# Performance work log

Hardware: AMD Instinct MI355X
Metric: run time of the kernel (lower is better)

The kernel has to match this reference:

```python
import jax, jax.numpy as jnp
import numpy as np

B, S, H = 8, 2048, 1024
NH, HD, NS, K = 16, 64, 64, 4  # num_heads, head_dim, state_size, conv kernel


def setup_inputs() -> dict:
    key = jax.random.key(0)
    ks = jax.random.split(key, 16)
    sc = 0.02
    return {
        "x": jax.random.normal(ks[0], (B, S, H), dtype=jnp.float32),
        # weights stored (in, out) so y = x @ W + b
        "in_proj_w": jax.random.normal(ks[1], (H, 2 * H), dtype=jnp.float32) * sc,
        "conv_w": jax.random.normal(ks[2], (H, 1, K), dtype=jnp.float32) * sc,
        "conv_b": jnp.zeros((H,), dtype=jnp.float32),
        "bb_w": jax.random.normal(ks[3], (HD, HD), dtype=jnp.float32) * sc,
        "bb_b": jnp.zeros((HD,), dtype=jnp.float32),
        "f1_w": jax.random.normal(ks[4], (HD, NS), dtype=jnp.float32) * sc,
        "f1_b": jnp.zeros((NS,), dtype=jnp.float32),
        "f2_w": jax.random.normal(ks[5], (HD, NS), dtype=jnp.float32) * sc,
        "f2_b": jnp.zeros((NS,), dtype=jnp.float32),
        "tau_a_w": jax.random.normal(ks[6], (HD, NS), dtype=jnp.float32) * sc,
        "tau_a_b": jnp.zeros((NS,), dtype=jnp.float32),
        "tau_b": jnp.zeros((NS,), dtype=jnp.float32),
        "decay_w": jax.random.normal(ks[7], (HD, NS), dtype=jnp.float32) * sc,
        "decay_b": jnp.zeros((NS,), dtype=jnp.float32),
        "state_out_w": jax.random.normal(ks[8], (NS, HD), dtype=jnp.float32) * sc,
        "state_out_b": jnp.zeros((HD,), dtype=jnp.float32),
        "out_proj_w": jax.random.normal(ks[9], (H, H), dtype=jnp.float32) * sc,
    }


def _short_conv(x, w, b):
    # x: (B,S,D) depthwise causal conv, kernel K, left-pad K-1
    xc = jnp.transpose(x, (0, 2, 1))  # (B,D,S)
    y = jax.lax.conv_general_dilated(
        xc, w, window_strides=(1,), padding=[(K - 1, 0)],
        feature_group_count=H, dimension_numbers=("NCH", "OIH", "NCH"))
    y = y + b[None, :, None]
    return jnp.transpose(y, (0, 2, 1))  # (B,S,D)


def _scan(decay, candidate):
    # decay, candidate: (B,S,NH,NS); h_t = d_t*h_{t-1} + (1-d_t)*c_t
    d = jnp.transpose(decay, (1, 0, 2, 3))      # (S,B,NH,NS)
    c = jnp.transpose(candidate, (1, 0, 2, 3))

    def step(h, dc):
        dt, ct = dc
        h = dt * h + (1.0 - dt) * ct
        return h, h

    h0 = jnp.zeros(d.shape[1:], dtype=decay.dtype)
    _, hs = jax.lax.scan(step, h0, (d, c))
    return jnp.transpose(hs, (1, 0, 2, 3))      # (B,S,NH,NS)


def reference(x, in_proj_w, conv_w, conv_b, bb_w, bb_b, f1_w, f1_b,
              f2_w, f2_b, tau_a_w, tau_a_b, tau_b, decay_w, decay_b,
              state_out_w, state_out_b, out_proj_w):
    xz = x @ in_proj_w                       # (B,S,2H)
    x_path, z_gate = jnp.split(xz, 2, axis=-1)
    x_path = jax.nn.silu(_short_conv(x_path, conv_w, conv_b))
    x_heads = x_path.reshape(B, S, NH, HD)
    bb = jax.nn.silu(x_heads @ bb_w + bb_b)  # backbone (1 layer)
    f1 = jnp.tanh(bb @ f1_w + f1_b)
    f2 = jnp.tanh(bb @ f2_w + f2_b)
    tau = jax.nn.sigmoid(bb @ tau_a_w + tau_a_b + tau_b)
    candidate = f1 * (1.0 - tau) + f2 * tau
    decay = jax.nn.sigmoid(bb @ decay_w + decay_b)
    h_seq = _scan(decay, candidate)          # (B,S,NH,NS)
    out = h_seq @ state_out_w + state_out_b  # (B,S,NH,HD)
    out = out.reshape(B, S, H)
    out = out * jax.nn.silu(z_gate)
    return out @ out_proj_w
```

## Files before the change

### kernel.cpp

```cpp
#include <hip/hip_runtime.h>
#include <hip/hip_bf16.h>
#include <math.h>

#define BN   8
#define SN   2048
#define HN   1024
#define NTOK 16384
#define NHD  16
#define HDD  64
#define NSD  64

typedef __attribute__((ext_vector_type(8))) short short8;
typedef __attribute__((ext_vector_type(4))) float f32x4;

__device__ __forceinline__ float fsig(float x)  { return 1.f / (1.f + __expf(-x)); }
__device__ __forceinline__ float fsilu(float x) { return x / (1.f + __expf(-x)); }
__device__ __forceinline__ float ftanh(float x) {
    const float t = __expf(-2.f * fabsf(x));
    const float r = (1.f - t) / (1.f + t);
    return x >= 0.f ? r : -r;
}
__device__ __forceinline__ void hilo(float v, __hip_bfloat16& h, __hip_bfloat16& l) {
    h = __float2bfloat16(v);
    l = __float2bfloat16(v - __bfloat162float(h));
}
__device__ __forceinline__ unsigned pack_cd(float cand, float dec) {
    __hip_bfloat16 cb_ = __float2bfloat16(cand);
    __hip_bfloat16 db_ = __float2bfloat16(dec);
    return (unsigned)*(unsigned short*)&cb_ | ((unsigned)*(unsigned short*)&db_ << 16);
}
__device__ __forceinline__ void gload_lds16(const void* g, void* l) {
    __builtin_amdgcn_global_load_lds(
        (const __attribute__((address_space(1))) unsigned int*)g,
        (__attribute__((address_space(3))) unsigned int*)l, 16, 0, 0);
}

__global__ __launch_bounds__(256)
void x_to_a_bf(const float* __restrict__ X, __hip_bfloat16* __restrict__ A)
{
    const int idx = blockIdx.x * 256 + threadIdx.x;
    const int r = idx >> 7;
    const int c = idx & 127;
    const float* src = &X[(size_t)r * 1024 + c * 8];
    alignas(16) __hip_bfloat16 b[8];
#pragma unroll
    for (int j = 0; j < 8; ++j) b[j] = __float2bfloat16(src[j]);
    const int cs = (c & 120) | ((c & 7) ^ (r & 7));
    *(short8*)&A[(size_t)r * 1024 + cs * 8] = *(const short8*)b;
}

__global__ __launch_bounds__(256)
void w_to_bt_bf(const float* __restrict__ W, __hip_bfloat16* __restrict__ BT, int N)
{
    __shared__ float t[64][65];
    const int k0 = blockIdx.x * 64;
    const int n0 = blockIdx.y * 64;
    const int c  = threadIdx.x & 63, r4 = threadIdx.x >> 6;
#pragma unroll
    for (int rr = 0; rr < 64; rr += 4)
        t[rr + r4][c] = W[(size_t)(k0 + rr + r4) * N + n0 + c];
    __syncthreads();
#pragma unroll
    for (int oo = 0; oo < 2; ++oo) {
        const int o = r4 * 2 + oo;
        alignas(16) __hip_bfloat16 b[8];
#pragma unroll
        for (int j = 0; j < 8; ++j)
            b[j] = __float2bfloat16(t[o * 8 + j][c]);
        const int n = n0 + c;
        const int cglob = (k0 >> 3) + o;
        const int cs = (cglob & 120) | ((cglob & 7) ^ (n & 7));
        *(short8*)&BT[(size_t)n * 1024 + cs * 8] = *(const short8*)b;
    }
}

__global__ __launch_bounds__(256)
void w5_to_wt(const float* __restrict__ w0, const float* __restrict__ w1,
              const float* __restrict__ w2, const float* __restrict__ w3,
              const float* __restrict__ w4, __hip_bfloat16* __restrict__ WT5)
{
    const int idx = blockIdx.x * 256 + threadIdx.x;
    if (idx >= 2560) return;
    const int o = idx & 7, n = (idx >> 3) & 63, mat = idx >> 9;
    const float* W = mat == 0 ? w0 : mat == 1 ? w1 : mat == 2 ? w2 : mat == 3 ? w3 : w4;
    alignas(16) __hip_bfloat16 hb[8], lb[8];
#pragma unroll
    for (int j = 0; j < 8; ++j) {
        const float v = W[(o * 8 + j) * 64 + n];
        hilo(v, hb[j], lb[j]);
    }
    __hip_bfloat16* row = WT5 + (size_t)(mat * 64 + n) * 128;
    *(short8*)&row[((o     ) ^ (n & 15)) * 8] = *(const short8*)hb;
    *(short8*)&row[((o | 8) ^ (n & 15)) * 8] = *(const short8*)lb;
}

template<int NCT, int MODE>
__global__ __launch_bounds__(512, 2)
void mfma_gemm256(const __hip_bfloat16* __restrict__ A,
                  const __hip_bfloat16* __restrict__ BT,
                  float* __restrict__ out0, float* __restrict__ out1)
{
    __shared__ __hip_bfloat16 lds[2][2][16384];
    const int tid  = threadIdx.x;
    const int lane = tid & 63, wave = tid >> 6;
    const int wr   = wave >> 2, wc = wave & 3;
    const int l15  = lane & 15, l4 = lane >> 4;

    const int nwg = gridDim.x;
    const int cpx = nwg >> 3;
    const int swz = (blockIdx.x & 7) * cpx + (blockIdx.x >> 3);
    const int mt = swz / NCT, nt = swz % NCT;
    const int row0 = mt * 256, col0 = nt * 256;

    const int s_c = tid & 7;
    const int s_r = (tid >> 3) & 63;

    f32x4 acc[8][4];
#pragma unroll
    for (int m = 0; m < 8; ++m)
#pragma unroll
        for (int n = 0; n < 4; ++n) acc[m][n] = (f32x4)0.f;

#define STAGE_I(I, TT, BUF)                                                    \
    {                                                                          \
        const int mat_ = (I) >> 2;                                             \
        const int row_ = ((I) & 3) * 64 + s_r;                                 \
        const __hip_bfloat16* src_ = (mat_ == 0)                               \
            ? &A [(size_t)(row0 + row_) * 1024 + ((TT) << 6) + s_c * 8]        \
            : &BT[(size_t)(col0 + row_) * 1024 + ((TT) << 6) + s_c * 8];       \
        gload_lds16(src_, &lds[BUF][mat_][row_ * 64 + s_c * 8]);               \
    }

#pragma unroll
    for (int i = 0; i < 8; ++i) STAGE_I(i, 0, 0)
    __syncthreads();

    for (int t = 0; t < 16; ++t) {
        const int cur = t & 1, nxt = cur ^ 1;
        const bool pf = (t < 15);

#pragma unroll
        for (int ks = 0; ks < 2; ++ks) {
            if (pf) {
#pragma unroll
                for (int i = ks * 4; i < ks * 4 + 4; ++i) STAGE_I(i, t + 1, nxt)
            }

            short8 af[8], bf[4];
#pragma unroll
            for (int m = 0; m < 8; ++m) {
                const int row = wr * 128 + m * 16 + l15;
                const int ch = (ks * 4 + l4) ^ (l15 & 7);
                af[m] = *(const short8*)&lds[cur][0][row * 64 + ch * 8];
            }
#pragma unroll
            for (int n = 0; n < 4; ++n) {
                const int row = wc * 64 + n * 16 + l15;
                const int ch = (ks * 4 + l4) ^ (l15 & 7);
                bf[n] = *(const short8*)&lds[cur][1][row * 64 + ch * 8];
            }

            __builtin_amdgcn_s_setprio(1);
#pragma unroll
            for (int m = 0; m < 8; ++m)
#pragma unroll
                for (int n = 0; n < 4; ++n)
                    acc[m][n] = __builtin_amdgcn_mfma_f32_16x16x32_bf16(af[m], bf[n], acc[m][n], 0, 0, 0);
            __builtin_amdgcn_s_setprio(0);
        }
        __syncthreads();
    }
#undef STAGE_I

    const int orow = l4 * 4, ocol = l15;
#pragma unroll
    for (int M = 0; M < 8; ++M)
#pragma unroll
        for (int N = 0; N < 4; ++N) {
            const int c = col0 + wc * 64 + N * 16 + ocol;
#pragma unroll
            for (int q = 0; q < 4; ++q) {
                const int r = row0 + wr * 128 + M * 16 + orow + q;
                const float v = acc[M][N][q];
                if (MODE == 0) {
                    out0[(size_t)r * (NCT * 256) + c] = v;
                } else {
                    if (c < 1024) out0[(size_t)r * 1024 + c] = v;
                    else          out1[(size_t)r * 1024 + (c - 1024)] = fsilu(v);
                }
            }
        }
}

__global__ __launch_bounds__(512, 1)
void backbone_mfma(const float* __restrict__ xpath,
                   const float* __restrict__ cw, const float* __restrict__ cb,
                   const __hip_bfloat16* __restrict__ WT5,
                   const float* __restrict__ bbb,
                   const float* __restrict__ f1b, const float* __restrict__ f2b,
                   const float* __restrict__ taub, const float* __restrict__ taub2,
                   const float* __restrict__ decb,
                   unsigned* __restrict__ cd)
{
    __shared__ __hip_bfloat16 Wl[5 * 64 * 128];
    __shared__ __hip_bfloat16 Xl[128 * 128];
    __shared__ __hip_bfloat16 Bb[128 * 128];
    const int tid  = threadIdx.x;
    const int lane = tid & 63, wave = tid >> 6;
    const int l15  = lane & 15, l4 = lane >> 4;

#pragma unroll
    for (int r = 0; r < 10; ++r) {
        const int blk = r * 8 + wave;
        gload_lds16(WT5 + blk * 512 + lane * 8, Wl + blk * 512);
    }

    {
        const int bt = blockIdx.x * 8 + wave;
        const int t  = bt & (SN - 1);
#pragma unroll
        for (int gg = 0; gg < 2; ++gg) {
            const int g  = lane + gg * 64;
            const int c0 = g * 8;
            float acc[8];
#pragma unroll
            for (int j = 0; j < 8; ++j) acc[j] = cb[c0 + j];
            float4 cwv[8];
#pragma unroll
            for (int j = 0; j < 8; ++j) cwv[j] = *(const float4*)&cw[(c0 + j) * 4];
            const float* cwf = (const float*)cwv;
#pragma unroll
            for (int k = 0; k < 4; ++k) {
                if (t - 3 + k >= 0) {
                    const float* xr = xpath + (((size_t)(bt - 3 + k)) << 10) + c0;
                    const float4 u0 = *(const float4*)&xr[0];
                    const float4 u1 = *(const float4*)&xr[4];
                    const float u[8] = {u0.x, u0.y, u0.z, u0.w, u1.x, u1.y, u1.z, u1.w};
#pragma unroll
                    for (int j = 0; j < 8; ++j) acc[j] += cwf[j * 4 + k] * u[j];
                }
            }
            alignas(16) __hip_bfloat16 hb[8], lb[8];
#pragma unroll
            for (int j = 0; j < 8; ++j) hilo(fsilu(acc[j]), hb[j], lb[j]);
            const int head = c0 >> 6;
            const int o    = (c0 >> 3) & 7;
            __hip_bfloat16* row = Xl + (wave * 16 + head) * 128;
            *(short8*)&row[((o     ) ^ head) * 8] = *(const short8*)hb;
            *(short8*)&row[((o | 8) ^ head) * 8] = *(const short8*)lb;
        }
    }
    __syncthreads();

    short8 xa[2][2];
#pragma unroll
    for (int s = 0; s < 2; ++s)
#pragma unroll
        for (int p = 0; p < 2; ++p) {
            const int ch = ((s * 4 + l4) | (p << 3)) ^ l15;
            xa[s][p] = *(const short8*)&Xl[(wave * 16 + l15) * 128 + ch * 8];
        }

#pragma unroll
    for (int nt = 0; nt < 4; ++nt) {
        short8 wb[2][2];
#pragma unroll
        for (int s = 0; s < 2; ++s)
#pragma unroll
            for (int p = 0; p < 2; ++p) {
                const int ch = ((s * 4 + l4) | (p << 3)) ^ l15;
                wb[s][p] = *(const short8*)&Wl[(nt * 16 + l15) * 128 + ch * 8];
            }
        f32x4 ac = (f32x4)0.f;
        __builtin_amdgcn_s_setprio(1);
#pragma unroll
        for (int s = 0; s < 2; ++s) {
            ac = __builtin_amdgcn_mfma_f32_16x16x32_bf16(xa[s][0], wb[s][0], ac, 0, 0, 0);
            ac = __builtin_amdgcn_mfma_f32_16x16x32_bf16(xa[s][0], wb[s][1], ac, 0, 0, 0);
            ac = __builtin_amdgcn_mfma_f32_16x16x32_bf16(xa[s][1], wb[s][0], ac, 0, 0, 0);
        }
        __builtin_amdgcn_s_setprio(0);
        const int col = nt * 16 + l15;
        const float bc = bbb[col];
#pragma unroll
        for (int q = 0; q < 4; ++q) {
            const int r15 = l4 * 4 + q;
            const float v = fsilu(ac[q] + bc);
            __hip_bfloat16 h, l;
            hilo(v, h, l);
            Bb[(wave * 16 + r15) * 128 + (((col >> 3)     ) ^ r15) * 8 + (col & 7)] = h;
            Bb[(wave * 16 + r15) * 128 + (((col >> 3) | 8) ^ r15) * 8 + (col & 7)] = l;
        }
    }

    short8 ba[2][2];
#pragma unroll
    for (int s = 0; s < 2; ++s)
#pragma unroll
        for (int p = 0; p < 2; ++p) {
            const int ch = ((s * 4 + l4) | (p << 3)) ^ l15;
            ba[s][p] = *(const short8*)&Bb[(wave * 16 + l15) * 128 + ch * 8];
        }

#pragma unroll
    for (int nt = 0; nt < 4; ++nt) {
        f32x4 a2[4];
#pragma unroll
        for (int m = 0; m < 4; ++m) a2[m] = (f32x4)0.f;

#pragma unroll
        for (int mat = 0; mat < 4; ++mat) {
            short8 w2[2][2];
#pragma unroll
            for (int s = 0; s < 2; ++s)
#pragma unroll
                for (int p = 0; p < 2; ++p) {
                    const int ch = ((s * 4 + l4) | (p << 3)) ^ l15;
                    w2[s][p] = *(const short8*)&Wl[((mat + 1) * 64 + nt * 16 + l15) * 128 + ch * 8];
                }
            __builtin_amdgcn_s_setprio(1);
#pragma unroll
            for (int s = 0; s < 2; ++s) {
                a2[mat] = __builtin_amdgcn_mfma_f32_16x16x32_bf16(ba[s][0], w2[s][0], a2[mat], 0, 0, 0);
                a2[mat] = __builtin_amdgcn_mfma_f32_16x16x32_bf16(ba[s][0], w2[s][1], a2[mat], 0, 0, 0);
                a2[mat] = __builtin_amdgcn_mfma_f32_16x16x32_bf16(ba[s][1], w2[s][0], a2[mat], 0, 0, 0);
            }
            __builtin_amdgcn_s_setprio(0);
        }

        const int col = nt * 16 + l15;
        const float b1 = f1b[col], b2 = f2b[col];
        const float b3 = taub[col] + taub2[col], b4 = decb[col];
        const size_t Rbase = (size_t)blockIdx.x * 128 + wave * 16;
#pragma unroll
        for (int q = 0; q < 4; ++q) {
            const size_t R = Rbase + l4 * 4 + q;
            const float f1v = ftanh(a2[0][q] + b1);
            const float f2v = ftanh(a2[1][q] + b2);
            const float tv  = fsig (a2[2][q] + b3);
            const float dv  = fsig (a2[3][q] + b4);
            cd[R * 64 + col] = pack_cd(f1v * (1.f - tv) + f2v * tv, dv);
        }
    }
}

__global__ __launch_bounds__(256)
void scan_compose(const unsigned* __restrict__ cd,
                  float* __restrict__ Ach, float* __restrict__ Bch)
{
    const int idx = blockIdx.x * 256 + threadIdx.x;
    const int p  = idx & 1023;
    const int rest = idx >> 10;
    const int ch = rest & 63, b = rest >> 6;
    float A = 1.f, Bv = 0.f;
    const size_t base = ((size_t)(b * SN + ch * 32) << 10) + p;
    for (int t = 0; t < 32; ++t) {
        const unsigned u = cd[base + ((size_t)t << 10)];
        const float c = __uint_as_float(u << 16);
        const float d = __uint_as_float(u & 0xffff0000u);
        A  *= d;
        Bv  = d * Bv + (1.f - d) * c;
    }
    Ach[(ch << 13) + (b << 10) + p] = A;
    Bch[(ch << 13) + (b << 10) + p] = Bv;
}

__global__ __launch_bounds__(256)
void scan_chunks(const float* __restrict__ Ach, const float* __restrict__ Bch,
                 float* __restrict__ hstart)
{
    const int q = blockIdx.x * 256 + threadIdx.x;
    float h = 0.f;
    for (int ch = 0; ch < 64; ++ch) {
        hstart[(ch << 13) + q] = h;
        h = Ach[(ch << 13) + q] * h + Bch[(ch << 13) + q];
    }
}

__global__ __launch_bounds__(256)
void scan_apply(const unsigned* __restrict__ cd,
                const float* __restrict__ hstart, __hip_bfloat16* __restrict__ Hhl)
{
    const int idx = blockIdx.x * 256 + threadIdx.x;
    const int p  = idx & 1023;
    const int rest = idx >> 10;
    const int ch = rest & 63, b = rest >> 6;
    const int nh = p >> 6, ns = p & 63;
    const int hoff = (((ns >> 3)    ) ^ nh) * 8 + (ns & 7);
    const int loff = (((ns >> 3) | 8) ^ nh) * 8 + (ns & 7);
    float h = hstart[(ch << 13) + (b << 10) + p];
    const int t0 = b * SN + ch * 32;
    const size_t base = ((size_t)t0 << 10) + p;
    for (int t = 0; t < 32; ++t) {
        const unsigned u = cd[base + ((size_t)t << 10)];
        const float c = __uint_as_float(u << 16);
        const float d = __uint_as_float(u & 0xffff0000u);
        h = d * h + (1.f - d) * c;
        __hip_bfloat16 hb, lb;
        hilo(h, hb, lb);
        const size_t row = ((size_t)(t0 + t) * 16 + nh) * 128;
        Hhl[row + hoff] = hb;
        Hhl[row + loff] = lb;
    }
}

__global__ __launch_bounds__(256)
void stateout_mfma(const __hip_bfloat16* __restrict__ Hhl,
                   const float* __restrict__ sow, const float* __restrict__ sob,
                   const float* __restrict__ zs, __hip_bfloat16* __restrict__ gA)
{
    __shared__ __hip_bfloat16 Wl[64 * 128];
    __shared__ __hip_bfloat16 Hl[128 * 128];
    const int tid  = threadIdx.x;
    const int lane = tid & 63, wave = tid >> 6;
    const int l15  = lane & 15, l4 = lane >> 4;

    {
        const int n = tid & 63;
        const int ob = (tid >> 6) * 2;
#pragma unroll
        for (int oo = 0; oo < 2; ++oo) {
            const int o = ob + oo;
#pragma unroll
            for (int j = 0; j < 8; ++j) {
                const float v = sow[(o * 8 + j) * 64 + n];
                __hip_bfloat16 hb, lb;
                hilo(v, hb, lb);
                Wl[n * 128 + ((o       ^ (n & 15)) * 8 + j)] = hb;
                Wl[n * 128 + (((o | 8) ^ (n & 15)) * 8 + j)] = lb;
            }
        }
    }
    const __hip_bfloat16* hsrc = Hhl + (size_t)blockIdx.x * 16384;
#pragma unroll
    for (int r = 0; r < 8; ++r) {
        const int blk = r * 4 + wave;
        gload_lds16(hsrc + blk * 512 + lane * 8, Hl + blk * 512);
    }
    __syncthreads();

    short8 ha[2][2][2];
#pragma unroll
    for (int mt2 = 0; mt2 < 2; ++mt2)
#pragma unroll
        for (int s = 0; s < 2; ++s)
#pragma unroll
            for (int p = 0; p < 2; ++p) {
                const int ch = ((s * 4 + l4) | (p << 3)) ^ l15;
                ha[mt2][s][p] = *(const short8*)&Hl[(wave * 32 + mt2 * 16 + l15) * 128 + ch * 8];
            }

#pragma unroll
    for (int nt = 0; nt < 4; ++nt) {
        short8 wb[2][2];
#pragma unroll
        for (int s = 0; s < 2; ++s)
#pragma unroll
            for (int p = 0; p < 2; ++p) {
                const int ch = ((s * 4 + l4) | (p << 3)) ^ l15;
                wb[s][p] = *(const short8*)&Wl[(nt * 16 + l15) * 128 + ch * 8];
            }
        f32x4 ac[2] = {(f32x4)0.f, (f32x4)0.f};
#pragma unroll
        for (int mt2 = 0; mt2 < 2; ++mt2)
#pragma unroll
            for (int s = 0; s < 2; ++s) {
                ac[mt2] = __builtin_amdgcn_mfma_f32_16x16x32_bf16(ha[mt2][s][0], wb[s][0], ac[mt2], 0, 0, 0);
                ac[mt2] = __builtin_amdgcn_mfma_f32_16x16x32_bf16(ha[mt2][s][0], wb[s][1], ac[mt2], 0, 0, 0);
                ac[mt2] = __builtin_amdgcn_mfma_f32_16x16x32_bf16(ha[mt2][s][1], wb[s][0], ac[mt2], 0, 0, 0);
            }
        const int col = nt * 16 + l15;
        const float bj = sob[col];
#pragma unroll
        for (int mt2 = 0; mt2 < 2; ++mt2)
#pragma unroll
            for (int q = 0; q < 4; ++q) {
                const size_t th = (size_t)blockIdx.x * 128 + wave * 32 + mt2 * 16 + l4 * 4 + q;
                const float v = (ac[mt2][q] + bj) * zs[th * 64 + col];
                const size_t token = th >> 4;
                const int colg = (int)(th & 15) * 64 + col;
                const int cg = colg >> 3, jg = colg & 7;
                const int cs = (cg & 120) | ((cg & 7) ^ ((int)(token & 7)));
                gA[token * 1024 + cs * 8 + jg] = __float2bfloat16(v);
            }
    }
}

extern "C" void kernel_launch(void* const* d_in, const int* in_sizes, int n_in,
                              void* d_out, int out_size, void* d_ws, size_t ws_size,
                              hipStream_t stream)
{
    const float* x     = (const float*)d_in[0];
    const float* ipw   = (const float*)d_in[1];
    const float* cw    = (const float*)d_in[2];
    const float* cb    = (const float*)d_in[3];
    const float* bbw   = (const float*)d_in[4];
    const float* bbb   = (const float*)d_in[5];
    const float* f1w   = (const float*)d_in[6];
    const float* f1b   = (const float*)d_in[7];
    const float* f2w   = (const float*)d_in[8];
    const float* f2b   = (const float*)d_in[9];
    const float* tauw  = (const float*)d_in[10];
    const float* taub  = (const float*)d_in[11];
    const float* taub2 = (const float*)d_in[12];
    const float* decw  = (const float*)d_in[13];
    const float* decb  = (const float*)d_in[14];
    const float* sow   = (const float*)d_in[15];
    const float* sob   = (const float*)d_in[16];
    const float* opw   = (const float*)d_in[17];

    float* out = (float*)d_out;
    char*  ws  = (char*)d_ws;
    const size_t MB = 1024 * 1024;

    __hip_bfloat16* Abf   = (__hip_bfloat16*)(ws);
    float*          xpath = (float*)(ws + 64 * MB);
    __hip_bfloat16* BTin  = (__hip_bfloat16*)(ws + 128 * MB);
    unsigned*       cd    = (unsigned*)(ws + 128 * MB);
    __hip_bfloat16* WT5   = (__hip_bfloat16*)(ws + 192 * MB);
    float*          Ach   = (float*)(ws + 192 * MB);
    float*          Bch   = Ach + 524288;
    float*          hst   = Bch + 524288;
    __hip_bfloat16* BTout = (__hip_bfloat16*)(ws + 192 * MB);
    __hip_bfloat16* Hhl   = (__hip_bfloat16*)(ws);
    __hip_bfloat16* gA    = (__hip_bfloat16*)(ws + 64 * MB);
    float*          zsilu = out;

    x_to_a_bf<<<8192, 256, 0, stream>>>(x, Abf);
    w_to_bt_bf<<<dim3(16, 32), 256, 0, stream>>>(ipw, BTin, 2048);
    w5_to_wt<<<10, 256, 0, stream>>>(bbw, f1w, f2w, tauw, decw, WT5);
    mfma_gemm256<8, 1><<<512, 512, 0, stream>>>(Abf, BTin, xpath, zsilu);
    backbone_mfma<<<2048, 512, 0, stream>>>(xpath, cw, cb, WT5, bbb, f1b, f2b,
                                            taub, taub2, decb, cd);
    scan_compose<<<2048, 256, 0, stream>>>(cd, Ach, Bch);
    scan_chunks<<<32, 256, 0, stream>>>(Ach, Bch, hst);
    scan_apply<<<2048, 256, 0, stream>>>(cd, hst, Hhl);
    w_to_bt_bf<<<dim3(16, 16), 256, 0, stream>>>(opw, BTout, 1024);
    stateout_mfma<<<2048, 256, 0, stream>>>(Hhl, sow, sob, zsilu, gA);
    mfma_gemm256<4, 0><<<256, 512, 0, stream>>>(gA, BTout, out, nullptr);
}
```

Measured before the change: 358.8 us.

## Drop hi/lo bf16 split in head-level GEMMs and split conv into own kernel

Removes the hi+lo bf16 error-compensation trick from the backbone, gate projections and state-out GEMMs. Each now uses plain bf16 operands, which halves the K dimension, cuts MFMA count by about a factor of three, halves LDS footprint and shrinks the Hhl intermediate. The depthwise conv+silu moves out of backbone_mfma into a separate elementwise kernel that writes a bf16 swizzled buffer, and occupancy hints are raised. The cost is lower numerical precision and an extra kernel launch with a round-trip through global memory.

```diff
diff --git a/kernel.cpp b/kernel.cpp
--- a/kernel.cpp
+++ b/kernel.cpp
@@ -20,10 +20,6 @@
     const float r = (1.f - t) / (1.f + t);
     return x >= 0.f ? r : -r;
 }
-__device__ __forceinline__ void hilo(float v, __hip_bfloat16& h, __hip_bfloat16& l) {
-    h = __float2bfloat16(v);
-    l = __float2bfloat16(v - __bfloat162float(h));
-}
 __device__ __forceinline__ unsigned pack_cd(float cand, float dec) {
     __hip_bfloat16 cb_ = __float2bfloat16(cand);
     __hip_bfloat16 db_ = __float2bfloat16(dec);
@@ -83,15 +79,11 @@
     if (idx >= 2560) return;
     const int o = idx & 7, n = (idx >> 3) & 63, mat = idx >> 9;
     const float* W = mat == 0 ? w0 : mat == 1 ? w1 : mat == 2 ? w2 : mat == 3 ? w3 : w4;
-    alignas(16) __hip_bfloat16 hb[8], lb[8];
-#pragma unroll
-    for (int j = 0; j < 8; ++j) {
-        const float v = W[(o * 8 + j) * 64 + n];
-        hilo(v, hb[j], lb[j]);
-    }
-    __hip_bfloat16* row = WT5 + (size_t)(mat * 64 + n) * 128;
-    *(short8*)&row[((o     ) ^ (n & 15)) * 8] = *(const short8*)hb;
-    *(short8*)&row[((o | 8) ^ (n & 15)) * 8] = *(const short8*)lb;
+    alignas(16) __hip_bfloat16 b[8];
+#pragma unroll
+    for (int j = 0; j < 8; ++j)
+        b[j] = __float2bfloat16(W[(o * 8 + j) * 64 + n]);
+    *(short8*)&WT5[(size_t)(mat * 64 + n) * 64 + ((o ^ (n & 7)) * 8)] = *(const short8*)b;
 }
 
 template<int NCT, int MODE>
@@ -192,9 +184,48 @@
         }
 }
 
-__global__ __launch_bounds__(512, 1)
-void backbone_mfma(const float* __restrict__ xpath,
-                   const float* __restrict__ cw, const float* __restrict__ cb,
+__global__ __launch_bounds__(256)
+void conv_silu_bf(const float* __restrict__ xp, const float* __restrict__ cw,
+                  const float* __restrict__ cb, __hip_bfloat16* __restrict__ Xbf)
+{
+    const int idx = blockIdx.x * 256 + threadIdx.x;
+    const int g  = idx & 127;
+    const int bt = idx >> 7;
+    const int t  = bt & (SN - 1);
+    const int c0 = g * 8;
+
+    float acc[8];
+#pragma unroll
+    for (int j = 0; j < 8; ++j) acc[j] = cb[c0 + j];
+    float4 cwv[8];
+#pragma unroll
+    for (int j = 0; j < 8; ++j) cwv[j] = *(const float4*)&cw[(c0 + j) * 4];
+    const float* cwf = (const float*)cwv;
+
+#pragma unroll
+    for (int k = 0; k < 4; ++k) {
+        if (t - 3 + k >= 0) {
+            const float* xr = xp + (((size_t)(bt - 3 + k)) << 10) + c0;
+            const float4 u0 = *(const float4*)&xr[0];
+            const float4 u1 = *(const float4*)&xr[4];
+            const float u[8] = {u0.x, u0.y, u0.z, u0.w, u1.x, u1.y, u1.z, u1.w};
+#pragma unroll
+            for (int j = 0; j < 8; ++j) acc[j] += cwf[j * 4 + k] * u[j];
+        }
+    }
+
+    alignas(16) __hip_bfloat16 b[8];
+#pragma unroll
+    for (int j = 0; j < 8; ++j) b[j] = __float2bfloat16(fsilu(acc[j]));
+
+    const int head = g >> 3;
+    const int o    = g & 7;
+    const size_t row = (size_t)bt * 16 + head;
+    *(short8*)&Xbf[row * 64 + ((o ^ (head & 7)) * 8)] = *(const short8*)b;
+}
+
+__global__ __launch_bounds__(512, 4)
+void backbone_mfma(const __hip_bfloat16* __restrict__ Xbf,
                    const __hip_bfloat16* __restrict__ WT5,
                    const float* __restrict__ bbb,
                    const float* __restrict__ f1b, const float* __restrict__ f2b,
@@ -202,105 +233,50 @@
                    const float* __restrict__ decb,
                    unsigned* __restrict__ cd)
 {
-    __shared__ __hip_bfloat16 Wl[5 * 64 * 128];
-    __shared__ __hip_bfloat16 Xl[128 * 128];
-    __shared__ __hip_bfloat16 Bb[128 * 128];
+    __shared__ __hip_bfloat16 Wl[5 * 64 * 64];
+    __shared__ __hip_bfloat16 Bb[128 * 64];
     const int tid  = threadIdx.x;
     const int lane = tid & 63, wave = tid >> 6;
     const int l15  = lane & 15, l4 = lane >> 4;
-
-#pragma unroll
-    for (int r = 0; r < 10; ++r) {
+    const int e7   = l15 & 7;
+
+#pragma unroll
+    for (int r = 0; r < 5; ++r) {
         const int blk = r * 8 + wave;
         gload_lds16(WT5 + blk * 512 + lane * 8, Wl + blk * 512);
     }
 
-    {
-        const int bt = blockIdx.x * 8 + wave;
-        const int t  = bt & (SN - 1);
-#pragma unroll
-        for (int gg = 0; gg < 2; ++gg) {
-            const int g  = lane + gg * 64;
-            const int c0 = g * 8;
-            float acc[8];
-#pragma unroll
-            for (int j = 0; j < 8; ++j) acc[j] = cb[c0 + j];
-            float4 cwv[8];
-#pragma unroll
-            for (int j = 0; j < 8; ++j) cwv[j] = *(const float4*)&cw[(c0 + j) * 4];
-            const float* cwf = (const float*)cwv;
-#pragma unroll
-            for (int k = 0; k < 4; ++k) {
-                if (t - 3 + k >= 0) {
-                    const float* xr = xpath + (((size_t)(bt - 3 + k)) << 10) + c0;
-                    const float4 u0 = *(const float4*)&xr[0];
-                    const float4 u1 = *(const float4*)&xr[4];
-                    const float u[8] = {u0.x, u0.y, u0.z, u0.w, u1.x, u1.y, u1.z, u1.w};
-#pragma unroll
-                    for (int j = 0; j < 8; ++j) acc[j] += cwf[j * 4 + k] * u[j];
-                }
-            }
-            alignas(16) __hip_bfloat16 hb[8], lb[8];
-#pragma unroll
-            for (int j = 0; j < 8; ++j) hilo(fsilu(acc[j]), hb[j], lb[j]);
-            const int head = c0 >> 6;
-            const int o    = (c0 >> 3) & 7;
-            __hip_bfloat16* row = Xl + (wave * 16 + head) * 128;
-            *(short8*)&row[((o     ) ^ head) * 8] = *(const short8*)hb;
-            *(short8*)&row[((o | 8) ^ head) * 8] = *(const short8*)lb;
-        }
-    }
+    const __hip_bfloat16* xrow = Xbf + ((size_t)(blockIdx.x * 8 + wave) * 16) * 64;
+    short8 xa[2];
+#pragma unroll
+    for (int s = 0; s < 2; ++s)
+        xa[s] = *(const short8*)&xrow[l15 * 64 + (((s * 4 + l4) ^ e7) * 8)];
+
     __syncthreads();
 
-    short8 xa[2][2];
-#pragma unroll
-    for (int s = 0; s < 2; ++s)
-#pragma unroll
-        for (int p = 0; p < 2; ++p) {
-            const int ch = ((s * 4 + l4) | (p << 3)) ^ l15;
-            xa[s][p] = *(const short8*)&Xl[(wave * 16 + l15) * 128 + ch * 8];
-        }
-
 #pragma unroll
     for (int nt = 0; nt < 4; ++nt) {
-        short8 wb[2][2];
+        short8 wb[2];
 #pragma unroll
         for (int s = 0; s < 2; ++s)
-#pragma unroll
-            for (int p = 0; p < 2; ++p) {
-                const int ch = ((s * 4 + l4) | (p << 3)) ^ l15;
-                wb[s][p] = *(const short8*)&Wl[(nt * 16 + l15) * 128 + ch * 8];
-            }
+            wb[s] = *(const short8*)&Wl[(nt * 16 + l15) * 64 + (((s * 4 + l4) ^ e7) * 8)];
         f32x4 ac = (f32x4)0.f;
-        __builtin_amdgcn_s_setprio(1);
-#pragma unroll
-        for (int s = 0; s < 2; ++s) {
-            ac = __builtin_amdgcn_mfma_f32_16x16x32_bf16(xa[s][0], wb[s][0], ac, 0, 0, 0);
-            ac = __builtin_amdgcn_mfma_f32_16x16x32_bf16(xa[s][0], wb[s][1], ac, 0, 0, 0);
-            ac = __builtin_amdgcn_mfma_f32_16x16x32_bf16(xa[s][1], wb[s][0], ac, 0, 0, 0);
-        }
-        __builtin_amdgcn_s_setprio(0);
+        ac = __builtin_amdgcn_mfma_f32_16x16x32_bf16(xa[0], wb[0], ac, 0, 0, 0);
+        ac = __builtin_amdgcn_mfma_f32_16x16x32_bf16(xa[1], wb[1], ac, 0, 0, 0);
         const int col = nt * 16 + l15;
         const float bc = bbb[col];
 #pragma unroll
         for (int q = 0; q < 4; ++q) {
             const int r15 = l4 * 4 + q;
-            const float v = fsilu(ac[q] + bc);
-            __hip_bfloat16 h, l;
-            hilo(v, h, l);
-            Bb[(wave * 16 + r15) * 128 + (((col >> 3)     ) ^ r15) * 8 + (col & 7)] = h;
-            Bb[(wave * 16 + r15) * 128 + (((col >> 3) | 8) ^ r15) * 8 + (col & 7)] = l;
-        }
-    }
-
-    short8 ba[2][2];
+            Bb[(wave * 16 + r15) * 64 + ((col >> 3) ^ (r15 & 7)) * 8 + (col & 7)] =
+                __float2bfloat16(fsilu(ac[q] + bc));
+        }
+    }
+
+    short8 ba[2];
 #pragma unroll
     for (int s = 0; s < 2; ++s)
-#pragma unroll
-        for (int p = 0; p < 2; ++p) {
-            const int ch = ((s * 4 + l4) | (p << 3)) ^ l15;
-            ba[s][p] = *(const short8*)&Bb[(wave * 16 + l15) * 128 + ch * 8];
-        }
+        ba[s] = *(const short8*)&Bb[(wave * 16 + l15) * 64 + (((s * 4 + l4) ^ e7) * 8)];
 
 #pragma unroll
     for (int nt = 0; nt < 4; ++nt) {
@@ -310,22 +286,12 @@
 
 #pragma unroll
         for (int mat = 0; mat < 4; ++mat) {
-            short8 w2[2][2];
+            short8 w2[2];
 #pragma unroll
             for (int s = 0; s < 2; ++s)
-#pragma unroll
-                for (int p = 0; p < 2; ++p) {
-                    const int ch = ((s * 4 + l4) | (p << 3)) ^ l15;
-                    w2[s][p] = *(const short8*)&Wl[((mat + 1) * 64 + nt * 16 + l15) * 128 + ch * 8];
-                }
-            __builtin_amdgcn_s_setprio(1);
-#pragma unroll
-            for (int s = 0; s < 2; ++s) {
-                a2[mat] = __builtin_amdgcn_mfma_f32_16x16x32_bf16(ba[s][0], w2[s][0], a2[mat], 0, 0, 0);
-                a2[mat] = __builtin_amdgcn_mfma_f32_16x16x32_bf16(ba[s][0], w2[s][1], a2[mat], 0, 0, 0);
-                a2[mat] = __builtin_amdgcn_mfma_f32_16x16x32_bf16(ba[s][1], w2[s][0], a2[mat], 0, 0, 0);
-            }
-            __builtin_amdgcn_s_setprio(0);
+                w2[s] = *(const short8*)&Wl[((mat + 1) * 64 + nt * 16 + l15) * 64 + (((s * 4 + l4) ^ e7) * 8)];
+            a2[mat] = __builtin_amdgcn_mfma_f32_16x16x32_bf16(ba[0], w2[0], a2[mat], 0, 0, 0);
+            a2[mat] = __builtin_amdgcn_mfma_f32_16x16x32_bf16(ba[1], w2[1], a2[mat], 0, 0, 0);
         }
 
         const int col = nt * 16 + l15;
@@ -386,8 +352,7 @@
     const int rest = idx >> 10;
     const int ch = rest & 63, b = rest >> 6;
     const int nh = p >> 6, ns = p & 63;
-    const int hoff = (((ns >> 3)    ) ^ nh) * 8 + (ns & 7);
-    const int loff = (((ns >> 3) | 8) ^ nh) * 8 + (ns & 7);
+    const int hpos = ((ns >> 3) ^ (nh & 7)) * 8 + (ns & 7);
     float h = hstart[(ch << 13) + (b << 10) + p];
     const int t0 = b * SN + ch * 32;
     const size_t base = ((size_t)t0 << 10) + p;
@@ -396,79 +361,62 @@
         const float c = __uint_as_float(u << 16);
         const float d = __uint_as_float(u & 0xffff0000u);
         h = d * h + (1.f - d) * c;
-        __hip_bfloat16 hb, lb;
-        hilo(h, hb, lb);
-        const size_t row = ((size_t)(t0 + t) * 16 + nh) * 128;
-        Hhl[row + hoff] = hb;
-        Hhl[row + loff] = lb;
-    }
-}
-
-__global__ __launch_bounds__(256)
+        Hhl[((size_t)(t0 + t) * 16 + nh) * 64 + hpos] = __float2bfloat16(h);
+    }
+}
+
+__global__ __launch_bounds__(256, 4)
 void stateout_mfma(const __hip_bfloat16* __restrict__ Hhl,
                    const float* __restrict__ sow, const float* __restrict__ sob,
                    const float* __restrict__ zs, __hip_bfloat16* __restrict__ gA)
 {
-    __shared__ __hip_bfloat16 Wl[64 * 128];
-    __shared__ __hip_bfloat16 Hl[128 * 128];
+    __shared__ __hip_bfloat16 Wl[64 * 64];
+    __shared__ __hip_bfloat16 Hl[128 * 64];
     const int tid  = threadIdx.x;
     const int lane = tid & 63, wave = tid >> 6;
     const int l15  = lane & 15, l4 = lane >> 4;
+    const int e7   = l15 & 7;
 
     {
         const int n = tid & 63;
-        const int ob = (tid >> 6) * 2;
+        const int o0 = tid >> 6;
 #pragma unroll
         for (int oo = 0; oo < 2; ++oo) {
-            const int o = ob + oo;
-#pragma unroll
-            for (int j = 0; j < 8; ++j) {
-                const float v = sow[(o * 8 + j) * 64 + n];
-                __hip_bfloat16 hb, lb;
-                hilo(v, hb, lb);
-                Wl[n * 128 + ((o       ^ (n & 15)) * 8 + j)] = hb;
-                Wl[n * 128 + (((o | 8) ^ (n & 15)) * 8 + j)] = lb;
-            }
-        }
-    }
-    const __hip_bfloat16* hsrc = Hhl + (size_t)blockIdx.x * 16384;
-#pragma unroll
-    for (int r = 0; r < 8; ++r) {
+            const int o = o0 + oo * 4;
+            alignas(16) __hip_bfloat16 b[8];
+#pragma unroll
+            for (int j = 0; j < 8; ++j)
+                b[j] = __float2bfloat16(sow[(o * 8 + j) * 64 + n]);
+            *(short8*)&Wl[n * 64 + ((o ^ (n & 7)) * 8)] = *(const short8*)b;
+        }
+    }
+    const __hip_bfloat16* hsrc = Hhl + (size_t)blockIdx.x * 8192;
+#pragma unroll
+    for (int r = 0; r < 4; ++r) {
         const int blk = r * 4 + wave;
         gload_lds16(hsrc + blk * 512 + lane * 8, Hl + blk * 512);
     }
     __syncthreads();
 
-    short8 ha[2][2][2];
+    short8 ha[2][2];
 #pragma unroll
     for (int mt2 = 0; mt2 < 2; ++mt2)
 #pragma unroll
         for (int s = 0; s < 2; ++s)
-#pragma unroll
-            for (int p = 0; p < 2; ++p) {
-                const int ch = ((s * 4 + l4) | (p << 3)) ^ l15;
-                ha[mt2][s][p] = *(const short8*)&Hl[(wave * 32 + mt2 * 16 + l15) * 128 + ch * 8];
-            }
+            ha[mt2][s] = *(const short8*)&Hl[(wave * 32 + mt2 * 16 + l15) * 64 + (((s * 4 + l4) ^ e7) * 8)];
 
 #pragma unroll
     for (int nt = 0; nt < 4; ++nt) {
-        short8 wb[2][2];
+        short8 wb[2];
 #pragma unroll
         for (int s = 0; s < 2; ++s)
-#pragma unroll
-            for (int p = 0; p < 2; ++p) {
-                const int ch = ((s * 4 + l4) | (p << 3)) ^ l15;
-                wb[s][p] = *(const short8*)&Wl[(nt * 16 + l15) * 128 + ch * 8];
-            }
+            wb[s] = *(const short8*)&Wl[(nt * 16 + l15) * 64 + (((s * 4 + l4) ^ e7) * 8)];
         f32x4 ac[2] = {(f32x4)0.f, (f32x4)0.f};
 #pragma unroll
-        for (int mt2 = 0; mt2 < 2; ++mt2)
-#pragma unroll
-            for (int s = 0; s < 2; ++s) {
-                ac[mt2] = __builtin_amdgcn_mfma_f32_16x16x32_bf16(ha[mt2][s][0], wb[s][0], ac[mt2], 0, 0, 0);
-                ac[mt2] = __builtin_amdgcn_mfma_f32_16x16x32_bf16(ha[mt2][s][0], wb[s][1], ac[mt2], 0, 0, 0);
-                ac[mt2] = __builtin_amdgcn_mfma_f32_16x16x32_bf16(ha[mt2][s][1], wb[s][0], ac[mt2], 0, 0, 0);
-            }
+        for (int mt2 = 0; mt2 < 2; ++mt2) {
+            ac[mt2] = __builtin_amdgcn_mfma_f32_16x16x32_bf16(ha[mt2][0], wb[0], ac[mt2], 0, 0, 0);
+            ac[mt2] = __builtin_amdgcn_mfma_f32_16x16x32_bf16(ha[mt2][1], wb[1], ac[mt2], 0, 0, 0);
+        }
         const int col = nt * 16 + l15;
         const float bj = sob[col];
 #pragma unroll
@@ -514,7 +462,10 @@
     const size_t MB = 1024 * 1024;
 
     __hip_bfloat16* Abf   = (__hip_bfloat16*)(ws);
+    __hip_bfloat16* Xbf   = (__hip_bfloat16*)(ws);
+    __hip_bfloat16* Hhl   = (__hip_bfloat16*)(ws + 32 * MB);
     float*          xpath = (float*)(ws + 64 * MB);
+    __hip_bfloat16* gA    = (__hip_bfloat16*)(ws + 64 * MB);
     __hip_bfloat16* BTin  = (__hip_bfloat16*)(ws + 128 * MB);
     unsigned*       cd    = (unsigned*)(ws + 128 * MB);
     __hip_bfloat16* WT5   = (__hip_bfloat16*)(ws + 192 * MB);
@@ -522,15 +473,14 @@
     float*          Bch   = Ach + 524288;
     float*          hst   = Bch + 524288;
     __hip_bfloat16* BTout = (__hip_bfloat16*)(ws + 192 * MB);
-    __hip_bfloat16* Hhl   = (__hip_bfloat16*)(ws);
-    __hip_bfloat16* gA    = (__hip_bfloat16*)(ws + 64 * MB);
     float*          zsilu = out;
 
     x_to_a_bf<<<8192, 256, 0, stream>>>(x, Abf);
     w_to_bt_bf<<<dim3(16, 32), 256, 0, stream>>>(ipw, BTin, 2048);
     w5_to_wt<<<10, 256, 0, stream>>>(bbw, f1w, f2w, tauw, decw, WT5);
     mfma_gemm256<8, 1><<<512, 512, 0, stream>>>(Abf, BTin, xpath, zsilu);
-    backbone_mfma<<<2048, 512, 0, stream>>>(xpath, cw, cb, WT5, bbb, f1b, f2b,
+    conv_silu_bf<<<8192, 256, 0, stream>>>(xpath, cw, cb, Xbf);
+    backbone_mfma<<<2048, 512, 0, stream>>>(Xbf, WT5, bbb, f1b, f2b,
                                             taub, taub2, decb, cd);
     scan_compose<<<2048, 256, 0, stream>>>(cd, Ach, Bch);
     scan_chunks<<<32, 256, 0, stream>>>(Ach, Bch, hst);
```

New measurement: 320.8 us. 10.6% less time.
